# Kernel tuning notes

Measured on AMD Instinct MI355X. Metric: run time of the kernel, lower is better.

Reference implementation:

```python
import jax, jax.numpy as jnp
import numpy as np

V, H, O = 32, 256, 256  # input_dim, hidden_dim, output_dim
EPS = 1e-5


def _layer_norm(x, g, b):
    m = jnp.mean(x, axis=-1, keepdims=True)
    v = jnp.mean((x - m) ** 2, axis=-1, keepdims=True)
    return g * (x - m) * jax.lax.rsqrt(v + EPS) + b


def setup_inputs() -> dict:
    key = jax.random.key(0)
    ks = jax.random.split(key, 20)
    s = 0.05
    inp = {
        "x": jax.random.normal(ks[0], (16, 256, V), dtype=jnp.float32),
        # selection GRN (input_dim -> input_dim, identity skip)
        "sel_fc1_w": jax.random.normal(ks[1], (V, H), dtype=jnp.float32) * s,
        "sel_fc1_b": jnp.zeros((H,), jnp.float32),
        "sel_fc2_w": jax.random.normal(ks[2], (H, V), dtype=jnp.float32) * s,
        "sel_fc2_b": jnp.zeros((V,), jnp.float32),
        "sel_gate_w": jax.random.normal(ks[3], (V, 2 * V), dtype=jnp.float32) * s,
        "sel_gate_b": jnp.zeros((2 * V,), jnp.float32),
        "sel_ln_g": jnp.ones((V,), jnp.float32),
        "sel_ln_b": jnp.zeros((V,), jnp.float32),
        # per-variable GRNs, stacked over the V variables (each has in_dim=1)
        "var_fc1_w": jax.random.normal(ks[4], (V, H), dtype=jnp.float32) * s,
        "var_fc1_b": jnp.zeros((V, H), jnp.float32),
        "var_fc2_w": jax.random.normal(ks[5], (V, H, O), dtype=jnp.float32) * s,
        "var_fc2_b": jnp.zeros((V, O), jnp.float32),
        "var_gate_w": jax.random.normal(ks[6], (V, 2 * O), dtype=jnp.float32) * s,
        "var_gate_b": jnp.zeros((V, 2 * O), jnp.float32),
        "var_skip_w": jax.random.normal(ks[7], (V, O), dtype=jnp.float32) * s,
        "var_skip_b": jnp.zeros((V, O), jnp.float32),
        "var_ln_g": jnp.ones((V, O), jnp.float32),
        "var_ln_b": jnp.zeros((V, O), jnp.float32),
    }
    return inp


def _vsn_forward(x, sel_fc1_w, sel_fc1_b, sel_fc2_w, sel_fc2_b, sel_gate_w,
                 sel_gate_b, sel_ln_g, sel_ln_b, var_fc1_w, var_fc1_b,
                 var_fc2_w, var_fc2_b, var_gate_w, var_gate_b, var_skip_w,
                 var_skip_b, var_ln_g, var_ln_b):
    B, S, _ = x.shape
    xr = x.reshape(-1, V)  # [N, V]

    # --- selection GRN (skip is identity) ---
    h = jax.nn.elu(xr @ sel_fc1_w + sel_fc1_b)        # [N, H]
    h = h @ sel_fc2_w + sel_fc2_b                      # [N, V] (unused by residual; matches torch code)
    g = xr @ sel_gate_w + sel_gate_b                   # [N, 2V]
    gates, values = jnp.split(g, 2, axis=-1)
    glu = jax.nn.sigmoid(gates) * values               # [N, V]
    sel = _layer_norm(glu + xr, sel_ln_g, sel_ln_b)    # [N, V]
    weights = jax.nn.softmax(sel, axis=-1)             # [N, V]

    # --- batched per-variable GRNs (in_dim = 1) ---
    xv = xr[..., None]                                  # [N, V, 1]
    hv = jax.nn.elu(xv * var_fc1_w + var_fc1_b)         # [N, V, H]
    hv = jnp.einsum('nvh,vho->nvo', hv, var_fc2_w) + var_fc2_b  # [N, V, O]
    gv = xv * var_gate_w + var_gate_b                   # [N, V, 2O]
    gates_v, values_v = jnp.split(gv, 2, axis=-1)
    glu_v = jax.nn.sigmoid(gates_v) * values_v          # [N, V, O]
    skip_v = xv * var_skip_w + var_skip_b               # [N, V, O]
    proc = _layer_norm(glu_v + skip_v, var_ln_g, var_ln_b)  # [N, V, O]

    out = jnp.einsum('nv,nvo->no', weights, proc)       # [N, O]
    return out.reshape(B, S, O)


def reference(x, sel_fc1_w, sel_fc1_b, sel_fc2_w, sel_fc2_b, sel_gate_w,
              sel_gate_b, sel_ln_g, sel_ln_b, var_fc1_w, var_fc1_b,
              var_fc2_w, var_fc2_b, var_gate_w, var_gate_b, var_skip_w,
              var_skip_b, var_ln_g, var_ln_b):
    return _vsn_forward(x, sel_fc1_w, sel_fc1_b, sel_fc2_w, sel_fc2_b,
                        sel_gate_w, sel_gate_b, sel_ln_g, sel_ln_b,
                        var_fc1_w, var_fc1_b, var_fc2_w, var_fc2_b,
                        var_gate_w, var_gate_b, var_skip_w, var_skip_b,
                        var_ln_g, var_ln_b)
```

## Files before the change

kernel.cpp:

```cpp
#include <hip/hip_runtime.h>
#include <hip/hip_bf16.h>


#define VDIM 32
#define ODIM 256
#define RPB  16
#define TPB  1024
#define CHUNK_V 2
#define NCHUNK  16

__device__ __forceinline__ float fast_sigmoid(float g) {
    return __builtin_amdgcn_rcpf(1.0f + __expf(-g));
}

__global__ void __launch_bounds__(TPB) vsn_fused(
    const float* __restrict__ x,
    const float* __restrict__ sgw,
    const float* __restrict__ sgb,
    const float* __restrict__ slg,
    const float* __restrict__ slb,
    const float* __restrict__ vgw,
    const float* __restrict__ vgb,
    const float* __restrict__ vsw,
    const float* __restrict__ vsb,
    const float* __restrict__ vlg,
    const float* __restrict__ vlb,
    float* __restrict__ out)
{
    __shared__ float wbuf[2][4096];
    __shared__ float x_s[RPB][VDIM];
    __shared__ float g_s[RPB][2 * VDIM];
    __shared__ float w_s[RPB][VDIM];

    const int tid  = threadIdx.x;
    const int row0 = blockIdx.x * RPB;

    const float* sbase;
    int sstr;
    if (tid < 256)      { sbase = vgw + (tid << 2);         sstr = 1024; }
    else if (tid < 512) { sbase = vgb + ((tid - 256) << 2); sstr = 1024; }
    else if (tid < 640) { sbase = vsw + ((tid - 512) << 2); sstr = 512;  }
    else if (tid < 768) { sbase = vsb + ((tid - 640) << 2); sstr = 512;  }
    else if (tid < 896) { sbase = vlg + ((tid - 768) << 2); sstr = 512;  }
    else                { sbase = vlb + ((tid - 896) << 2); sstr = 512;  }

    const float4 st0 = *(const float4*)sbase;

    if (tid < RPB * VDIM)
        ((float*)x_s)[tid] = x[row0 * VDIM + tid];
    __syncthreads();

    {
        const int r = tid >> 6, j = tid & 63;
        float acc = sgb[j];
        #pragma unroll
        for (int v = 0; v < VDIM; ++v)
            acc = fmaf(x_s[r][v], sgw[v * 64 + j], acc);
        g_s[r][j] = acc;
    }
    __syncthreads();

    ((float4*)wbuf[0])[tid & 1023] = st0;

    if (tid < RPB * VDIM) {
        const int r = tid >> 5, v = tid & 31;
        const float gate = g_s[r][v];
        const float val  = g_s[r][VDIM + v];
        const float y    = fast_sigmoid(gate) * val + x_s[r][v];
        float s1 = y, s2 = y * y;
        #pragma unroll
        for (int m = 1; m < 32; m <<= 1) {
            s1 += __shfl_xor(s1, m, 64);
            s2 += __shfl_xor(s2, m, 64);
        }
        const float mean = s1 * (1.0f / VDIM);
        const float var  = s2 * (1.0f / VDIM) - mean * mean;
        const float rs   = __builtin_amdgcn_rsqf(var + 1e-5f);
        const float sel  = slg[v] * ((y - mean) * rs) + slb[v];
        float mx = sel;
        #pragma unroll
        for (int m = 1; m < 32; m <<= 1)
            mx = fmaxf(mx, __shfl_xor(mx, m, 64));
        const float e = __expf(sel - mx);
        float se = e;
        #pragma unroll
        for (int m = 1; m < 32; m <<= 1)
            se += __shfl_xor(se, m, 64);
        w_s[r][v] = e * __builtin_amdgcn_rcpf(se);
    }
    __syncthreads();

    const int wave = tid >> 6;
    const int lane = tid & 63;
    const int o0   = lane << 2;

    float acc0 = 0.0f, acc1 = 0.0f, acc2 = 0.0f, acc3 = 0.0f;

    for (int c = 0; c < NCHUNK; ++c) {
        float4 pf;
        if (c < NCHUNK - 1)
            pf = *(const float4*)(sbase + (c + 1) * sstr);

        const float* buf = wbuf[c & 1];

        #pragma unroll
        for (int v4 = 0; v4 < CHUNK_V; ++v4) {
            const int v = c * CHUNK_V + v4;
            const float4 ga  = *(const float4*)(buf + v4 * 512 + o0);
            const float4 va  = *(const float4*)(buf + v4 * 512 + 256 + o0);
            const float4 gab = *(const float4*)(buf + 1024 + v4 * 512 + o0);
            const float4 vab = *(const float4*)(buf + 1024 + v4 * 512 + 256 + o0);
            const float4 sw4 = *(const float4*)(buf + 2048 + v4 * 256 + o0);
            const float4 sb4 = *(const float4*)(buf + 2560 + v4 * 256 + o0);
            const float4 lg4 = *(const float4*)(buf + 3072 + v4 * 256 + o0);
            const float4 lb4 = *(const float4*)(buf + 3584 + v4 * 256 + o0);

            const float xv = x_s[wave][v];

            const float y0 = fast_sigmoid(fmaf(xv, ga.x, gab.x)) * fmaf(xv, va.x, vab.x) + fmaf(xv, sw4.x, sb4.x);
            const float y1 = fast_sigmoid(fmaf(xv, ga.y, gab.y)) * fmaf(xv, va.y, vab.y) + fmaf(xv, sw4.y, sb4.y);
            const float y2 = fast_sigmoid(fmaf(xv, ga.z, gab.z)) * fmaf(xv, va.z, vab.z) + fmaf(xv, sw4.z, sb4.z);
            const float y3 = fast_sigmoid(fmaf(xv, ga.w, gab.w)) * fmaf(xv, va.w, vab.w) + fmaf(xv, sw4.w, sb4.w);

            float s1 = (y0 + y1) + (y2 + y3);
            float s2 = fmaf(y0, y0, fmaf(y1, y1, fmaf(y2, y2, y3 * y3)));
            #pragma unroll
            for (int m = 1; m < 64; m <<= 1) {
                s1 += __shfl_xor(s1, m, 64);
                s2 += __shfl_xor(s2, m, 64);
            }
            const float mean = s1 * (1.0f / ODIM);
            const float var  = s2 * (1.0f / ODIM) - mean * mean;
            const float rs   = __builtin_amdgcn_rsqf(var + 1e-5f);
            const float wv   = w_s[wave][v];
            const float wrs  = wv * rs;
            acc0 = fmaf(lg4.x, (y0 - mean) * wrs, fmaf(wv, lb4.x, acc0));
            acc1 = fmaf(lg4.y, (y1 - mean) * wrs, fmaf(wv, lb4.y, acc1));
            acc2 = fmaf(lg4.z, (y2 - mean) * wrs, fmaf(wv, lb4.z, acc2));
            acc3 = fmaf(lg4.w, (y3 - mean) * wrs, fmaf(wv, lb4.w, acc3));
        }

        if (c < NCHUNK - 1)
            ((float4*)wbuf[(c + 1) & 1])[tid & 1023] = pf;
        __syncthreads();
    }

    float4 o4 = make_float4(acc0, acc1, acc2, acc3);
    *(float4*)(out + (size_t)(row0 + wave) * ODIM + o0) = o4;
}

extern "C" void kernel_launch(void* const* d_in, const int* in_sizes, int n_in,
                              void* d_out, int out_size, void* d_ws, size_t ws_size,
                              hipStream_t stream) {
    const float* x   = (const float*)d_in[0];
    const float* sgw = (const float*)d_in[5];
    const float* sgb = (const float*)d_in[6];
    const float* slg = (const float*)d_in[7];
    const float* slb = (const float*)d_in[8];
    const float* vgw = (const float*)d_in[13];
    const float* vgb = (const float*)d_in[14];
    const float* vsw = (const float*)d_in[15];
    const float* vsb = (const float*)d_in[16];
    const float* vlg = (const float*)d_in[17];
    const float* vlb = (const float*)d_in[18];
    float* out = (float*)d_out;

    const int N = in_sizes[0] / VDIM;
    const int grid = N / RPB;

    vsn_fused<<<grid, TPB, 0, stream>>>(x, sgw, sgb, slg, slb,
                                        vgw, vgb, vsw, vsb, vlg, vlb, out);
}
```

Measured before the change: 125.2 us.

## Shrink blocks, process two rows per wave, use DPP wave reductions

The block shrinks from 1024 to 256 threads covering 8 rows, so each wave now handles two rows. Every weight float4 read from LDS is reused for both rows, which halves LDS traffic per output. Each thread now stages four float4s per chunk instead of one, and the block count doubles. The per-row LayerNorm sum reductions move from shfl_xor butterflies to a DPP row-shift/broadcast scan followed by a readlane, which cuts cross-lane instruction cost. The trade-off is higher register pressure from the second row's accumulators and the extra prefetch registers.

Result: slower. 134.3 us (+7.3%).

```diff
diff --git a/kernel.cpp b/kernel.cpp
--- a/kernel.cpp
+++ b/kernel.cpp
@@ -4,16 +4,33 @@
 
 #define VDIM 32
 #define ODIM 256
-#define RPB  16
-#define TPB  1024
-#define CHUNK_V 2
-#define NCHUNK  16
+#define RPB  8
+#define TPB  256
+#define NCHUNK 16
 
 __device__ __forceinline__ float fast_sigmoid(float g) {
     return __builtin_amdgcn_rcpf(1.0f + __expf(-g));
 }
 
-__global__ void __launch_bounds__(TPB) vsn_fused(
+template <int CTRL>
+__device__ __forceinline__ float dpp_add(float x) {
+    int s = __builtin_amdgcn_update_dpp(0, __builtin_bit_cast(int, x),
+                                        CTRL, 0xF, 0xF, true);
+    return x + __builtin_bit_cast(float, s);
+}
+
+__device__ __forceinline__ float wave_sum(float x) {
+    x = dpp_add<0x111>(x);
+    x = dpp_add<0x112>(x);
+    x = dpp_add<0x114>(x);
+    x = dpp_add<0x118>(x);
+    x = dpp_add<0x142>(x);
+    x = dpp_add<0x143>(x);
+    return __builtin_bit_cast(float,
+        __builtin_amdgcn_readlane(__builtin_bit_cast(int, x), 63));
+}
+
+__global__ void __launch_bounds__(TPB, 2) vsn_fused(
     const float* __restrict__ x,
     const float* __restrict__ sgw,
     const float* __restrict__ sgb,
@@ -35,23 +52,24 @@
     const int tid  = threadIdx.x;
     const int row0 = blockIdx.x * RPB;
 
-    const float* sbase;
-    int sstr;
-    if (tid < 256)      { sbase = vgw + (tid << 2);         sstr = 1024; }
-    else if (tid < 512) { sbase = vgb + ((tid - 256) << 2); sstr = 1024; }
-    else if (tid < 640) { sbase = vsw + ((tid - 512) << 2); sstr = 512;  }
-    else if (tid < 768) { sbase = vsb + ((tid - 640) << 2); sstr = 512;  }
-    else if (tid < 896) { sbase = vlg + ((tid - 768) << 2); sstr = 512;  }
-    else                { sbase = vlb + ((tid - 896) << 2); sstr = 512;  }
-
-    const float4 st0 = *(const float4*)sbase;
-
-    if (tid < RPB * VDIM)
-        ((float*)x_s)[tid] = x[row0 * VDIM + tid];
+    const float* sb[4];
+    int ss[4];
+    sb[0] = vgw + (tid << 2);                       ss[0] = 1024;
+    sb[1] = vgb + (tid << 2);                       ss[1] = 1024;
+    sb[2] = ((tid < 128) ? vsw : (vsb - 512)) + ((tid + 512 - 512) << 2); ss[2] = 512;
+    sb[3] = ((tid < 128) ? vlg : (vlb - 512)) + ((tid + 768 - 768) << 2); ss[3] = 512;
+
+    float4 st0[4];
+    #pragma unroll
+    for (int k = 0; k < 4; ++k) st0[k] = *(const float4*)sb[k];
+
+    ((float*)x_s)[tid] = x[row0 * VDIM + tid];
     __syncthreads();
 
-    {
-        const int r = tid >> 6, j = tid & 63;
+    #pragma unroll
+    for (int it = 0; it < 2; ++it) {
+        const int i = tid + it * TPB;
+        const int r = i >> 6, j = i & 63;
         float acc = sgb[j];
         #pragma unroll
         for (int v = 0; v < VDIM; ++v)
@@ -60,9 +78,11 @@
     }
     __syncthreads();
 
-    ((float4*)wbuf[0])[tid & 1023] = st0;
-
-    if (tid < RPB * VDIM) {
+    #pragma unroll
+    for (int k = 0; k < 4; ++k)
+        ((float4*)wbuf[0])[tid + k * TPB] = st0[k];
+
+    {
         const int r = tid >> 5, v = tid & 31;
         const float gate = g_s[r][v];
         const float val  = g_s[r][VDIM + v];
@@ -93,19 +113,24 @@
     const int wave = tid >> 6;
     const int lane = tid & 63;
     const int o0   = lane << 2;
-
-    float acc0 = 0.0f, acc1 = 0.0f, acc2 = 0.0f, acc3 = 0.0f;
+    const int rA   = wave * 2, rB = rA + 1;
+
+    float aA0 = 0.f, aA1 = 0.f, aA2 = 0.f, aA3 = 0.f;
+    float aB0 = 0.f, aB1 = 0.f, aB2 = 0.f, aB3 = 0.f;
 
     for (int c = 0; c < NCHUNK; ++c) {
-        float4 pf;
-        if (c < NCHUNK - 1)
-            pf = *(const float4*)(sbase + (c + 1) * sstr);
+        float4 pf[4];
+        if (c < NCHUNK - 1) {
+            #pragma unroll
+            for (int k = 0; k < 4; ++k)
+                pf[k] = *(const float4*)(sb[k] + (c + 1) * ss[k]);
+        }
 
         const float* buf = wbuf[c & 1];
 
         #pragma unroll
-        for (int v4 = 0; v4 < CHUNK_V; ++v4) {
-            const int v = c * CHUNK_V + v4;
+        for (int v4 = 0; v4 < 2; ++v4) {
+            const int v = c * 2 + v4;
             const float4 ga  = *(const float4*)(buf + v4 * 512 + o0);
             const float4 va  = *(const float4*)(buf + v4 * 512 + 256 + o0);
             const float4 gab = *(const float4*)(buf + 1024 + v4 * 512 + o0);
@@ -115,38 +140,54 @@
             const float4 lg4 = *(const float4*)(buf + 3072 + v4 * 256 + o0);
             const float4 lb4 = *(const float4*)(buf + 3584 + v4 * 256 + o0);
 
-            const float xv = x_s[wave][v];
-
-            const float y0 = fast_sigmoid(fmaf(xv, ga.x, gab.x)) * fmaf(xv, va.x, vab.x) + fmaf(xv, sw4.x, sb4.x);
-            const float y1 = fast_sigmoid(fmaf(xv, ga.y, gab.y)) * fmaf(xv, va.y, vab.y) + fmaf(xv, sw4.y, sb4.y);
-            const float y2 = fast_sigmoid(fmaf(xv, ga.z, gab.z)) * fmaf(xv, va.z, vab.z) + fmaf(xv, sw4.z, sb4.z);
-            const float y3 = fast_sigmoid(fmaf(xv, ga.w, gab.w)) * fmaf(xv, va.w, vab.w) + fmaf(xv, sw4.w, sb4.w);
-
-            float s1 = (y0 + y1) + (y2 + y3);
-            float s2 = fmaf(y0, y0, fmaf(y1, y1, fmaf(y2, y2, y3 * y3)));
+            const float xa = x_s[rA][v];
+            const float xb = x_s[rB][v];
+
+            const float yA0 = fast_sigmoid(fmaf(xa, ga.x, gab.x)) * fmaf(xa, va.x, vab.x) + fmaf(xa, sw4.x, sb4.x);
+            const float yA1 = fast_sigmoid(fmaf(xa, ga.y, gab.y)) * fmaf(xa, va.y, vab.y) + fmaf(xa, sw4.y, sb4.y);
+            const float yA2 = fast_sigmoid(fmaf(xa, ga.z, gab.z)) * fmaf(xa, va.z, vab.z) + fmaf(xa, sw4.z, sb4.z);
+            const float yA3 = fast_sigmoid(fmaf(xa, ga.w, gab.w)) * fmaf(xa, va.w, vab.w) + fmaf(xa, sw4.w, sb4.w);
+            const float yB0 = fast_sigmoid(fmaf(xb, ga.x, gab.x)) * fmaf(xb, va.x, vab.x) + fmaf(xb, sw4.x, sb4.x);
+            const float yB1 = fast_sigmoid(fmaf(xb, ga.y, gab.y)) * fmaf(xb, va.y, vab.y) + fmaf(xb, sw4.y, sb4.y);
+            const float yB2 = fast_sigmoid(fmaf(xb, ga.z, gab.z)) * fmaf(xb, va.z, vab.z) + fmaf(xb, sw4.z, sb4.z);
+            const float yB3 = fast_sigmoid(fmaf(xb, ga.w, gab.w)) * fmaf(xb, va.w, vab.w) + fmaf(xb, sw4.w, sb4.w);
+
+            const float s1a = wave_sum((yA0 + yA1) + (yA2 + yA3));
+            const float s2a = wave_sum(fmaf(yA0, yA0, fmaf(yA1, yA1, fmaf(yA2, yA2, yA3 * yA3))));
+            const float s1b = wave_sum((yB0 + yB1) + (yB2 + yB3));
+            const float s2b = wave_sum(fmaf(yB0, yB0, fmaf(yB1, yB1, fmaf(yB2, yB2, yB3 * yB3))));
+
+            const float mA = s1a * (1.0f / ODIM);
+            const float vA = s2a * (1.0f / ODIM) - mA * mA;
+            const float rsA = __builtin_amdgcn_rsqf(vA + 1e-5f);
+            const float wA = w_s[rA][v];
+            const float wrsA = wA * rsA;
+            aA0 = fmaf(lg4.x, (yA0 - mA) * wrsA, fmaf(wA, lb4.x, aA0));
+            aA1 = fmaf(lg4.y, (yA1 - mA) * wrsA, fmaf(wA, lb4.y, aA1));
+            aA2 = fmaf(lg4.z, (yA2 - mA) * wrsA, fmaf(wA, lb4.z, aA2));
+            aA3 = fmaf(lg4.w, (yA3 - mA) * wrsA, fmaf(wA, lb4.w, aA3));
+
+            const float mB = s1b * (1.0f / ODIM);
+            const float vB = s2b * (1.0f / ODIM) - mB * mB;
+            const float rsB = __builtin_amdgcn_rsqf(vB + 1e-5f);
+            const float wB = w_s[rB][v];
+            const float wrsB = wB * rsB;
+            aB0 = fmaf(lg4.x, (yB0 - mB) * wrsB, fmaf(wB, lb4.x, aB0));
+            aB1 = fmaf(lg4.y, (yB1 - mB) * wrsB, fmaf(wB, lb4.y, aB1));
+            aB2 = fmaf(lg4.z, (yB2 - mB) * wrsB, fmaf(wB, lb4.z, aB2));
+            aB3 = fmaf(lg4.w, (yB3 - mB) * wrsB, fmaf(wB, lb4.w, aB3));
+        }
+
+        if (c < NCHUNK - 1) {
             #pragma unroll
-            for (int m = 1; m < 64; m <<= 1) {
-                s1 += __shfl_xor(s1, m, 64);
-                s2 += __shfl_xor(s2, m, 64);
-            }
-            const float mean = s1 * (1.0f / ODIM);
-            const float var  = s2 * (1.0f / ODIM) - mean * mean;
-            const float rs   = __builtin_amdgcn_rsqf(var + 1e-5f);
-            const float wv   = w_s[wave][v];
-            const float wrs  = wv * rs;
-            acc0 = fmaf(lg4.x, (y0 - mean) * wrs, fmaf(wv, lb4.x, acc0));
-            acc1 = fmaf(lg4.y, (y1 - mean) * wrs, fmaf(wv, lb4.y, acc1));
-            acc2 = fmaf(lg4.z, (y2 - mean) * wrs, fmaf(wv, lb4.z, acc2));
-            acc3 = fmaf(lg4.w, (y3 - mean) * wrs, fmaf(wv, lb4.w, acc3));
-        }
-
-        if (c < NCHUNK - 1)
-            ((float4*)wbuf[(c + 1) & 1])[tid & 1023] = pf;
+            for (int k = 0; k < 4; ++k)
+                ((float4*)wbuf[(c + 1) & 1])[tid + k * TPB] = pf[k];
+        }
         __syncthreads();
     }
 
-    float4 o4 = make_float4(acc0, acc1, acc2, acc3);
-    *(float4*)(out + (size_t)(row0 + wave) * ODIM + o0) = o4;
+    *(float4*)(out + (size_t)(row0 + rA) * ODIM + o0) = make_float4(aA0, aA1, aA2, aA3);
+    *(float4*)(out + (size_t)(row0 + rB) * ODIM + o0) = make_float4(aB0, aB1, aB2, aB3);
 }
 
 extern "C" void kernel_launch(void* const* d_in, const int* in_sizes, int n_in,
```
